# Kernel tuning notes

Hardware: AMD Instinct MI355X
Metric: run time of the kernel (lower is better)

The kernel has to match this reference:

```python
import jax, jax.numpy as jnp
import numpy as np

VOCAB, DIM, B, S = 32000, 1024, 64, 512

def setup_inputs() -> dict:
    key = jax.random.key(0)
    ks = jax.random.split(key, 16)
    std = 1.0 / np.sqrt(DIM)
    return {
        "x": jax.random.randint(ks[0], (B,), 0, VOCAB),
        "h": jax.random.normal(ks[1], (B, DIM), jnp.float32),
        "c": jax.random.normal(ks[2], (B, DIM), jnp.float32),
        "enc_y": jax.random.normal(ks[3], (B, S, DIM), jnp.float32),
        "F_emb": jax.random.normal(ks[4], (VOCAB, DIM), jnp.float32),
        "W1_w": jax.random.uniform(ks[5], (DIM, DIM), jnp.float32, -std, std),
        "W1_b": jnp.zeros((DIM,), jnp.float32),
        "W2_w": jax.random.uniform(ks[6], (DIM, DIM), jnp.float32, -std, std),
        "W2_b": jnp.zeros((DIM,), jnp.float32),
        "V_w": jax.random.uniform(ks[7], (1, DIM), jnp.float32, -std, std),
        "V_b": jnp.zeros((1,), jnp.float32),
        "W_ih": jax.random.uniform(ks[8], (4 * DIM, DIM), jnp.float32, -std, std),
        "W_hh": jax.random.uniform(ks[9], (4 * DIM, DIM), jnp.float32, -std, std),
        "b_ih": jax.random.uniform(ks[10], (4 * DIM,), jnp.float32, -std, std),
        "b_hh": jax.random.uniform(ks[11], (4 * DIM,), jnp.float32, -std, std),
        "fc_w": jax.random.uniform(ks[12], (VOCAB, DIM), jnp.float32, -std, std),
        "fc_b": jnp.zeros((VOCAB,), jnp.float32),
    }

def reference(x, h, c, enc_y, F_emb, W1_w, W1_b, W2_w, W2_b, V_w, V_b,
              W_ih, W_hh, b_ih, b_hh, fc_w, fc_b):
    # Bahdanau additive attention (weights returned; context is dead code for layer=1)
    i_s = jnp.einsum('bsd,ed->bse', enc_y, W1_w) + W1_b          # [B,S,D]
    j_s = (h @ W2_w.T + W2_b)[:, None, :]                        # [B,1,D]
    score = jnp.tanh(i_s + j_s)                                  # [B,S,D]
    att = jax.nn.softmax(score @ V_w.T + V_b, axis=1)            # [B,S,1]
    # embedding lookup for the step token
    emb = F_emb[x]                                               # [B,D]
    # single-step LSTM (pytorch gate order: i, f, g, o)
    gates = emb @ W_ih.T + b_ih + h @ W_hh.T + b_hh              # [B,4D]
    ig, fg, gg, og = jnp.split(gates, 4, axis=-1)
    c_new = jax.nn.sigmoid(fg) * c + jax.nn.sigmoid(ig) * jnp.tanh(gg)
    h_new = jax.nn.sigmoid(og) * jnp.tanh(c_new)
    out = h_new + emb                                            # residual skip
    logits = out @ fc_w.T + fc_b                                 # [B,VOCAB]
    return logits, h_new, c_new, att
```

## Files before the change

kernel.cpp:

```cpp
#include <hip/hip_runtime.h>

#define DEV __device__ __forceinline__

typedef __bf16 bf16_t;
typedef bf16_t bf16x8 __attribute__((ext_vector_type(8)));
typedef float f32x4 __attribute__((ext_vector_type(4)));

static constexpr int VOCAB = 32000, DIM = 1024, BATCH = 64, SEQ = 512;
static constexpr int M_SC = BATCH * SEQ;

DEV unsigned short f2bf(float f) {
  unsigned u = __builtin_bit_cast(unsigned, f);
  u += 0x7FFFu + ((u >> 16) & 1u);
  return (unsigned short)(u >> 16);
}

DEV float sigmf(float x) {
  x = fminf(fmaxf(x, -30.f), 30.f);
  return 1.0f / (1.0f + __expf(-x));
}

DEV float tanh_fast(float x) {
  x = fminf(fmaxf(x, -20.f), 20.f);
  float e = __expf(2.0f * x);
  return (e - 1.0f) / (e + 1.0f);
}

DEV void gload_lds16(const void* g, void* l) {
  __builtin_amdgcn_global_load_lds(
      (__attribute__((address_space(1))) void*)(g),
      (__attribute__((address_space(3))) void*)(l), 16, 0, 0);
}

__global__ void __launch_bounds__(256) k_prep(const float* __restrict__ enc,
                                              const float* __restrict__ w1,
                                              unsigned short* __restrict__ enc_b,
                                              unsigned short* __restrict__ w1_b,
                                              float* __restrict__ att_l) {
  int gid = blockIdx.x * 256 + threadIdx.x;
  if (gid < M_SC) att_l[gid] = 0.f;
  const int ENC4 = (M_SC * DIM) / 4;
  const int TOT4 = ENC4 + (DIM * DIM) / 4;
  int stride = gridDim.x * 256;
  for (int i = gid; i < TOT4; i += stride) {
    float4 v;
    unsigned short* dst;
    if (i < ENC4) {
      v = ((const float4*)enc)[i];
      dst = enc_b + (size_t)i * 4;
    } else {
      v = ((const float4*)w1)[i - ENC4];
      dst = w1_b + (size_t)(i - ENC4) * 4;
    }
    ushort4 o;
    o.x = f2bf(v.x); o.y = f2bf(v.y); o.z = f2bf(v.z); o.w = f2bf(v.w);
    *(ushort4*)dst = o;
  }
}

__global__ void k_embed(const int* __restrict__ x, const float* __restrict__ Femb,
                        const float* __restrict__ h, float* __restrict__ emb_f,
                        unsigned short* __restrict__ eh_b, unsigned short* __restrict__ h_b) {
  int b = blockIdx.x;
  int tok = x[b];
  for (int d = threadIdx.x; d < DIM; d += blockDim.x) {
    float e = Femb[(size_t)tok * DIM + d];
    float hv = h[b * DIM + d];
    emb_f[b * DIM + d] = e;
    unsigned short eb = f2bf(e), hb = f2bf(hv);
    eh_b[b * 2 * DIM + d] = eb;
    eh_b[b * 2 * DIM + DIM + d] = hb;
    h_b[b * DIM + d] = hb;
  }
}

__global__ void __launch_bounds__(256) k_skinny(
    const unsigned short* __restrict__ A, int lda,
    const float* __restrict__ B1, const float* __restrict__ B2, int ksplit,
    const float* __restrict__ bias, float* __restrict__ C, int N, int K) {
  __shared__ unsigned short As[2][64 * 128];
  __shared__ unsigned short Bs[2][16 * 128];
  int t = threadIdx.x;
  int l = t & 63, w = t >> 6;
  int n0 = blockIdx.x * 16;
  f32x4 acc = {};
  int rx = (l & 7) << 3;

  float4 vB[2];

  auto loadB = [&](int k0) {
    const float* Bsrc;
    int kk;
    if (k0 < ksplit) { Bsrc = B1; kk = k0; } else { Bsrc = B2; kk = k0 - ksplit; }
#pragma unroll
    for (int i = 0; i < 2; ++i) {
      int lin = i * 256 + t;
      int row = lin >> 5, c4 = (lin & 31) * 4;
      vB[i] = *(const float4*)(Bsrc + (size_t)(n0 + row) * 1024 + kk + c4);
    }
  };
  auto writeB = [&](int bufi) {
#pragma unroll
    for (int i = 0; i < 2; ++i) {
      int lin = i * 256 + t;
      int row = lin >> 5, c4 = (lin & 31) * 4;
      ushort4 o;
      o.x = f2bf(vB[i].x); o.y = f2bf(vB[i].y); o.z = f2bf(vB[i].z); o.w = f2bf(vB[i].w);
      *(ushort4*)&Bs[bufi][row * 128 + (c4 ^ ((row & 7) << 3))] = o;
    }
  };
  auto stageA = [&](int k0, int bufi) {
#pragma unroll
    for (int i = 0; i < 4; ++i) {
      int sbase = i * 256 + w * 64;
      int s = sbase + l;
      int row = s >> 4;
      int scol = ((s & 15) ^ (row & 7)) * 8;
      gload_lds16(A + (size_t)row * lda + k0 + scol, &As[bufi][sbase * 8]);
    }
  };
  auto compute = [&](int bufi) {
#pragma unroll
    for (int kf = 0; kf < 4; ++kf) {
      int ko = kf * 32 + 8 * (l >> 4);
      int ar = w * 16 + (l & 15);
      bf16x8 af = *(const bf16x8*)&As[bufi][ar * 128 + (ko ^ rx)];
      bf16x8 bf = *(const bf16x8*)&Bs[bufi][(l & 15) * 128 + (ko ^ rx)];
      acc = __builtin_amdgcn_mfma_f32_16x16x32_bf16(af, bf, acc, 0, 0, 0);
    }
  };

  loadB(0);
  stageA(0, 0);
  writeB(0);
  asm volatile("s_waitcnt lgkmcnt(0)" ::: "memory");

  int nk = K / 128;
  int cur = 0;
  for (int kt = 0; kt < nk - 1; ++kt) {
    loadB((kt + 1) * 128);
    stageA((kt + 1) * 128, cur ^ 1);
    asm volatile("s_waitcnt vmcnt(6)\n\ts_barrier" ::: "memory");
    compute(cur);
    writeB(cur ^ 1);
    asm volatile("s_waitcnt lgkmcnt(0)\n\ts_barrier" ::: "memory");
    cur ^= 1;
  }
  asm volatile("s_waitcnt vmcnt(0)\n\ts_barrier" ::: "memory");
  compute(cur);

  int cn = n0 + (l & 15);
  float bv = bias ? bias[cn] : 0.f;
#pragma unroll
  for (int r = 0; r < 4; ++r) {
    int m = w * 16 + (l >> 4) * 4 + r;
    C[(size_t)m * N + cn] = acc[r] + bv;
  }
}

__global__ void __launch_bounds__(256) k_score(
    const unsigned short* __restrict__ encb, const unsigned short* __restrict__ w1mat,
    const float* __restrict__ js, const float* __restrict__ w1bias,
    const float* __restrict__ vw, float* __restrict__ att_l) {
  __shared__ unsigned short As[2][128 * 64];
  __shared__ unsigned short Bs[2][128 * 64];
  int t = threadIdx.x;
  int l = t & 63, w = t >> 6;
  int wr = w >> 1, wc = w & 1;
  int wg = blockIdx.x;
  int swz = (wg & 7) * 256 + (wg >> 3);
  int m0 = (swz >> 3) * 128;
  int n0 = (swz & 7) * 128;
  f32x4 acc[4][4] = {};

  int srow = l >> 3;
  int scol = ((l & 7) ^ (l >> 3)) * 8;
  int rx = (l & 7) << 3;

  const unsigned short* pa = encb + (size_t)m0 * DIM;
  const unsigned short* pb = w1mat + (size_t)n0 * DIM;

  auto stage = [&](int kt, int bufi) {
    int kbase = kt * 64;
#pragma unroll
    for (int i = 0; i < 4; ++i) {
      int chunk = i * 4 + w;
      int row = chunk * 8 + srow;
      gload_lds16(pa + (size_t)row * DIM + kbase + scol, &As[bufi][chunk * 512]);
      gload_lds16(pb + (size_t)row * DIM + kbase + scol, &Bs[bufi][chunk * 512]);
    }
  };
  auto compute = [&](int bufi) {
#pragma unroll
    for (int kh = 0; kh < 2; ++kh) {
      int ko = kh * 32 + 8 * (l >> 4);
      int kos = ko ^ rx;
      bf16x8 bfr[4], afr[4];
#pragma unroll
      for (int ni = 0; ni < 4; ++ni)
        bfr[ni] = *(const bf16x8*)&Bs[bufi][(wc * 64 + ni * 16 + (l & 15)) * 64 + kos];
#pragma unroll
      for (int mi = 0; mi < 4; ++mi)
        afr[mi] = *(const bf16x8*)&As[bufi][(wr * 64 + mi * 16 + (l & 15)) * 64 + kos];
      __builtin_amdgcn_s_setprio(1);
#pragma unroll
      for (int mi = 0; mi < 4; ++mi)
#pragma unroll
        for (int ni = 0; ni < 4; ++ni)
          acc[mi][ni] = __builtin_amdgcn_mfma_f32_16x16x32_bf16(afr[mi], bfr[ni], acc[mi][ni], 0, 0, 0);
      __builtin_amdgcn_s_setprio(0);
    }
  };

  stage(0, 0);
  int cur = 0;
  for (int kt = 0; kt < 15; ++kt) {
    stage(kt + 1, cur ^ 1);
    asm volatile("s_waitcnt vmcnt(8)\n\ts_barrier" ::: "memory");
    compute(cur);
    asm volatile("s_barrier" ::: "memory");
    cur ^= 1;
  }
  asm volatile("s_waitcnt vmcnt(0)\n\ts_barrier" ::: "memory");
  compute(cur);

  int b = m0 >> 9;
  const float* jrow = js + b * DIM;
  float psum[4][4] = {};
#pragma unroll
  for (int ni = 0; ni < 4; ++ni) {
    int e = n0 + wc * 64 + ni * 16 + (l & 15);
    float jv = jrow[e] + w1bias[e];
    float vv = vw[e];
#pragma unroll
    for (int mi = 0; mi < 4; ++mi)
#pragma unroll
      for (int r = 0; r < 4; ++r)
        psum[mi][r] += tanh_fast(acc[mi][ni][r] + jv) * vv;
  }
#pragma unroll
  for (int mi = 0; mi < 4; ++mi)
#pragma unroll
    for (int r = 0; r < 4; ++r) {
      float s = psum[mi][r];
      s += __shfl_xor(s, 1);
      s += __shfl_xor(s, 2);
      s += __shfl_xor(s, 4);
      s += __shfl_xor(s, 8);
      if ((l & 15) == 0)
        atomicAdd(&att_l[m0 + wr * 64 + mi * 16 + (l >> 4) * 4 + r], s);
    }
}

__global__ void k_softmax(const float* __restrict__ att_l, float* __restrict__ att) {
  __shared__ float red[16];
  int b = blockIdx.x, t = threadIdx.x;
  float v = att_l[b * SEQ + t];
  float m = v;
#pragma unroll
  for (int o = 32; o; o >>= 1) m = fmaxf(m, __shfl_xor(m, o));
  if ((t & 63) == 0) red[t >> 6] = m;
  __syncthreads();
  m = red[0];
#pragma unroll
  for (int i = 1; i < 8; ++i) m = fmaxf(m, red[i]);
  float e = __expf(v - m);
  float s = e;
#pragma unroll
  for (int o = 32; o; o >>= 1) s += __shfl_xor(s, o);
  __syncthreads();
  if ((t & 63) == 0) red[8 + (t >> 6)] = s;
  __syncthreads();
  s = 0.f;
#pragma unroll
  for (int i = 0; i < 8; ++i) s += red[8 + i];
  att[b * SEQ + t] = e / s;
}

__global__ void k_lstm(const float* __restrict__ gates, const float* __restrict__ bih,
                       const float* __restrict__ bhh, const float* __restrict__ c,
                       const float* __restrict__ emb_f, float* __restrict__ out_h,
                       float* __restrict__ out_c, unsigned short* __restrict__ out_b) {
  int t = blockIdx.x * 256 + threadIdx.x;
  int b = t >> 10, d = t & 1023;
  const float* g = gates + b * 4 * DIM;
  float ig = g[d] + bih[d] + bhh[d];
  float fg = g[DIM + d] + bih[DIM + d] + bhh[DIM + d];
  float gg = g[2 * DIM + d] + bih[2 * DIM + d] + bhh[2 * DIM + d];
  float og = g[3 * DIM + d] + bih[3 * DIM + d] + bhh[3 * DIM + d];
  float cn = sigmf(fg) * c[t] + sigmf(ig) * tanh_fast(gg);
  float hn = sigmf(og) * tanh_fast(cn);
  out_h[t] = hn;
  out_c[t] = cn;
  out_b[t] = f2bf(hn + emb_f[t]);
}

extern "C" void kernel_launch(void* const* d_in, const int* in_sizes, int n_in,
                              void* d_out, int out_size, void* d_ws, size_t ws_size,
                              hipStream_t stream) {
  const int* x = (const int*)d_in[0];
  const float* h = (const float*)d_in[1];
  const float* c = (const float*)d_in[2];
  const float* enc = (const float*)d_in[3];
  const float* Femb = (const float*)d_in[4];
  const float* W1w = (const float*)d_in[5];
  const float* W1b = (const float*)d_in[6];
  const float* W2w = (const float*)d_in[7];
  const float* W2b = (const float*)d_in[8];
  const float* Vw = (const float*)d_in[9];
  const float* Wih = (const float*)d_in[11];
  const float* Whh = (const float*)d_in[12];
  const float* bih = (const float*)d_in[13];
  const float* bhh = (const float*)d_in[14];
  const float* fcw = (const float*)d_in[15];
  const float* fcb = (const float*)d_in[16];

  float* out_logits = (float*)d_out;
  float* out_h = out_logits + (size_t)BATCH * VOCAB;
  float* out_c = out_h + BATCH * DIM;
  float* out_att = out_c + BATCH * DIM;

  char* p = (char*)d_ws;
  unsigned short* enc_b = (unsigned short*)p; p += (size_t)M_SC * DIM * 2;
  unsigned short* w1_b = (unsigned short*)p;  p += (size_t)DIM * DIM * 2;
  float* att_l = (float*)p;                   p += (size_t)M_SC * 4;
  float* js = (float*)p;                      p += (size_t)BATCH * DIM * 4;
  float* emb_f = (float*)p;                   p += (size_t)BATCH * DIM * 4;
  unsigned short* eh_b = (unsigned short*)p;  p += (size_t)BATCH * 2 * DIM * 2;
  unsigned short* h_b = (unsigned short*)p;   p += (size_t)BATCH * DIM * 2;
  float* gates = (float*)p;                   p += (size_t)BATCH * 4 * DIM * 4;
  unsigned short* out_b = (unsigned short*)p; p += (size_t)BATCH * DIM * 2;

  hipLaunchKernelGGL(k_prep, dim3(2048), dim3(256), 0, stream, enc, W1w, enc_b, w1_b, att_l);
  hipLaunchKernelGGL(k_embed, dim3(BATCH), dim3(256), 0, stream, x, Femb, h, emb_f, eh_b, h_b);
  hipLaunchKernelGGL(k_skinny, dim3(DIM / 16), dim3(256), 0, stream,
                     h_b, DIM, W2w, W2w, DIM, W2b, js, DIM, DIM);
  hipLaunchKernelGGL(k_score, dim3(2048), dim3(256), 0, stream,
                     enc_b, w1_b, js, W1b, Vw, att_l);
  hipLaunchKernelGGL(k_softmax, dim3(BATCH), dim3(SEQ), 0, stream, att_l, out_att);
  hipLaunchKernelGGL(k_skinny, dim3(4 * DIM / 16), dim3(256), 0, stream,
                     eh_b, 2 * DIM, Wih, Whh, DIM, (const float*)nullptr, gates, 4 * DIM, 2 * DIM);
  hipLaunchKernelGGL(k_lstm, dim3(BATCH * DIM / 256), dim3(256), 0, stream,
                     gates, bih, bhh, c, emb_f, out_h, out_c, out_b);
  hipLaunchKernelGGL(k_skinny, dim3(VOCAB / 16), dim3(256), 0, stream,
                     out_b, DIM, fcw, fcw, DIM, fcb, out_logits, VOCAB, DIM);
}
```

Measured before the change: 201.9 us.

## Fuse fp32-to-bf16 conversion of encoder states into score GEMM A-tile loads

The separate pass that converted the whole 32768x1024 encoder tensor to bf16 in workspace is removed. The score kernel now loads fp32 encoder rows into registers, converts them, and writes swizzled bf16 into LDS, software-pipelined one k-step ahead. The tile grows to 128x256 with 512 threads, so each fp32 A row is read from HBM four times instead of eight times as bf16. This saves the write and re-read of a 64MB intermediate, at the cost of more register pressure and VALU conversion work inside the GEMM loop.

```diff
diff --git a/kernel.cpp b/kernel.cpp
--- a/kernel.cpp
+++ b/kernel.cpp
@@ -32,30 +32,15 @@
       (__attribute__((address_space(3))) void*)(l), 16, 0, 0);
 }
 
-__global__ void __launch_bounds__(256) k_prep(const float* __restrict__ enc,
-                                              const float* __restrict__ w1,
-                                              unsigned short* __restrict__ enc_b,
-                                              unsigned short* __restrict__ w1_b,
-                                              float* __restrict__ att_l) {
+__global__ void __launch_bounds__(256) k_small(const float* __restrict__ w1,
+                                               unsigned short* __restrict__ w1_b,
+                                               float* __restrict__ att_l) {
   int gid = blockIdx.x * 256 + threadIdx.x;
   if (gid < M_SC) att_l[gid] = 0.f;
-  const int ENC4 = (M_SC * DIM) / 4;
-  const int TOT4 = ENC4 + (DIM * DIM) / 4;
-  int stride = gridDim.x * 256;
-  for (int i = gid; i < TOT4; i += stride) {
-    float4 v;
-    unsigned short* dst;
-    if (i < ENC4) {
-      v = ((const float4*)enc)[i];
-      dst = enc_b + (size_t)i * 4;
-    } else {
-      v = ((const float4*)w1)[i - ENC4];
-      dst = w1_b + (size_t)(i - ENC4) * 4;
-    }
-    ushort4 o;
-    o.x = f2bf(v.x); o.y = f2bf(v.y); o.z = f2bf(v.z); o.w = f2bf(v.w);
-    *(ushort4*)dst = o;
-  }
+  float4 v = ((const float4*)w1)[gid];
+  ushort4 o;
+  o.x = f2bf(v.x); o.y = f2bf(v.y); o.z = f2bf(v.z); o.w = f2bf(v.w);
+  *(ushort4*)(w1_b + (size_t)gid * 4) = o;
 }
 
 __global__ void k_embed(const int* __restrict__ x, const float* __restrict__ Femb,
@@ -158,97 +143,127 @@
   }
 }
 
-__global__ void __launch_bounds__(256) k_score(
-    const unsigned short* __restrict__ encb, const unsigned short* __restrict__ w1mat,
+__global__ void __launch_bounds__(512) k_score(
+    const float* __restrict__ enc, const unsigned short* __restrict__ w1mat,
     const float* __restrict__ js, const float* __restrict__ w1bias,
     const float* __restrict__ vw, float* __restrict__ att_l) {
   __shared__ unsigned short As[2][128 * 64];
-  __shared__ unsigned short Bs[2][128 * 64];
-  int t = threadIdx.x;
-  int l = t & 63, w = t >> 6;
-  int wr = w >> 1, wc = w & 1;
+  __shared__ unsigned short Bs[2][256 * 64];
+  int tid = threadIdx.x;
+  int lane = tid & 63, wid = tid >> 6;
+  int wr = wid >> 2, wn = wid & 3;
+  int lm = lane & 15, lq = lane >> 4;
+  int rx = (lane & 7) << 3;
+
   int wg = blockIdx.x;
-  int swz = (wg & 7) * 256 + (wg >> 3);
-  int m0 = (swz >> 3) * 128;
-  int n0 = (swz & 7) * 128;
+  int swz = (wg & 7) * 128 + (wg >> 3);
+  int m0 = (swz >> 2) * 128;
+  int n0 = (swz & 3) * 256;
+
   f32x4 acc[4][4] = {};
 
-  int srow = l >> 3;
-  int scol = ((l & 7) ^ (l >> 3)) * 8;
-  int rx = (l & 7) << 3;
-
-  const unsigned short* pa = encb + (size_t)m0 * DIM;
-  const unsigned short* pb = w1mat + (size_t)n0 * DIM;
-
-  auto stage = [&](int kt, int bufi) {
-    int kbase = kt * 64;
+  int arow[2], aq[2];
+#pragma unroll
+  for (int i = 0; i < 2; ++i) {
+    int lin = i * 512 + tid;
+    arow[i] = lin >> 3;
+    aq[i] = lin & 7;
+  }
+  float4 vA[2][2];
+  auto loadA = [&](int kb) {
+#pragma unroll
+    for (int i = 0; i < 2; ++i) {
+      const float* src = enc + (size_t)(m0 + arow[i]) * DIM + kb + aq[i] * 8;
+      vA[i][0] = *(const float4*)(src);
+      vA[i][1] = *(const float4*)(src + 4);
+    }
+  };
+  auto writeA = [&](int bufi) {
+#pragma unroll
+    for (int i = 0; i < 2; ++i) {
+      uint4 o;
+      o.x = (unsigned)f2bf(vA[i][0].x) | ((unsigned)f2bf(vA[i][0].y) << 16);
+      o.y = (unsigned)f2bf(vA[i][0].z) | ((unsigned)f2bf(vA[i][0].w) << 16);
+      o.z = (unsigned)f2bf(vA[i][1].x) | ((unsigned)f2bf(vA[i][1].y) << 16);
+      o.w = (unsigned)f2bf(vA[i][1].z) | ((unsigned)f2bf(vA[i][1].w) << 16);
+      *(uint4*)&As[bufi][arow[i] * 64 + ((aq[i] ^ (arow[i] & 7)) * 8)] = o;
+    }
+  };
+  auto stageB = [&](int kb, int bufi) {
 #pragma unroll
     for (int i = 0; i < 4; ++i) {
-      int chunk = i * 4 + w;
-      int row = chunk * 8 + srow;
-      gload_lds16(pa + (size_t)row * DIM + kbase + scol, &As[bufi][chunk * 512]);
-      gload_lds16(pb + (size_t)row * DIM + kbase + scol, &Bs[bufi][chunk * 512]);
+      int sbase = i * 512 + wid * 64;
+      int s = sbase + lane;
+      int brow = s >> 3, bq = s & 7;
+      int bcol = (bq ^ (brow & 7)) * 8;
+      gload_lds16(w1mat + (size_t)(n0 + brow) * DIM + kb + bcol, &Bs[bufi][sbase * 8]);
     }
   };
   auto compute = [&](int bufi) {
 #pragma unroll
-    for (int kh = 0; kh < 2; ++kh) {
-      int ko = kh * 32 + 8 * (l >> 4);
-      int kos = ko ^ rx;
-      bf16x8 bfr[4], afr[4];
-#pragma unroll
-      for (int ni = 0; ni < 4; ++ni)
-        bfr[ni] = *(const bf16x8*)&Bs[bufi][(wc * 64 + ni * 16 + (l & 15)) * 64 + kos];
-#pragma unroll
-      for (int mi = 0; mi < 4; ++mi)
-        afr[mi] = *(const bf16x8*)&As[bufi][(wr * 64 + mi * 16 + (l & 15)) * 64 + kos];
+    for (int kf = 0; kf < 2; ++kf) {
+      int kos = (kf * 32 + 8 * lq) ^ rx;
+      bf16x8 af[4], bfr[4];
+#pragma unroll
+      for (int mf = 0; mf < 4; ++mf)
+        af[mf] = *(const bf16x8*)&As[bufi][(wr * 64 + mf * 16 + lm) * 64 + kos];
+#pragma unroll
+      for (int nf = 0; nf < 4; ++nf)
+        bfr[nf] = *(const bf16x8*)&Bs[bufi][(wn * 64 + nf * 16 + lm) * 64 + kos];
       __builtin_amdgcn_s_setprio(1);
 #pragma unroll
-      for (int mi = 0; mi < 4; ++mi)
-#pragma unroll
-        for (int ni = 0; ni < 4; ++ni)
-          acc[mi][ni] = __builtin_amdgcn_mfma_f32_16x16x32_bf16(afr[mi], bfr[ni], acc[mi][ni], 0, 0, 0);
+      for (int mf = 0; mf < 4; ++mf)
+#pragma unroll
+        for (int nf = 0; nf < 4; ++nf)
+          acc[mf][nf] = __builtin_amdgcn_mfma_f32_16x16x32_bf16(af[mf], bfr[nf], acc[mf][nf], 0, 0, 0);
       __builtin_amdgcn_s_setprio(0);
     }
   };
 
-  stage(0, 0);
-  int cur = 0;
-  for (int kt = 0; kt < 15; ++kt) {
-    stage(kt + 1, cur ^ 1);
-    asm volatile("s_waitcnt vmcnt(8)\n\ts_barrier" ::: "memory");
-    compute(cur);
-    asm volatile("s_barrier" ::: "memory");
-    cur ^= 1;
-  }
-  asm volatile("s_waitcnt vmcnt(0)\n\ts_barrier" ::: "memory");
-  compute(cur);
+  loadA(0);
+  stageB(0, 0);
+  writeA(0);
+  asm volatile("s_waitcnt lgkmcnt(0)\n\ts_barrier" ::: "memory");
+
+  for (int t = 0; t < 16; ++t) {
+    int s = t & 1;
+    if (t < 15) {
+      loadA((t + 1) * 64);
+      stageB((t + 1) * 64, s ^ 1);
+      asm volatile("s_waitcnt vmcnt(8)\n\ts_barrier" ::: "memory");
+    } else {
+      asm volatile("s_waitcnt vmcnt(0)\n\ts_barrier" ::: "memory");
+    }
+    compute(s);
+    if (t < 15) writeA(s ^ 1);
+    asm volatile("s_waitcnt lgkmcnt(0)\n\ts_barrier" ::: "memory");
+  }
 
   int b = m0 >> 9;
   const float* jrow = js + b * DIM;
   float psum[4][4] = {};
 #pragma unroll
-  for (int ni = 0; ni < 4; ++ni) {
-    int e = n0 + wc * 64 + ni * 16 + (l & 15);
+  for (int nf = 0; nf < 4; ++nf) {
+    int e = n0 + wn * 64 + nf * 16 + lm;
     float jv = jrow[e] + w1bias[e];
     float vv = vw[e];
 #pragma unroll
-    for (int mi = 0; mi < 4; ++mi)
+    for (int mf = 0; mf < 4; ++mf)
 #pragma unroll
       for (int r = 0; r < 4; ++r)
-        psum[mi][r] += tanh_fast(acc[mi][ni][r] + jv) * vv;
-  }
-#pragma unroll
-  for (int mi = 0; mi < 4; ++mi)
+        psum[mf][r] += tanh_fast(acc[mf][nf][r] + jv) * vv;
+  }
+#pragma unroll
+  for (int mf = 0; mf < 4; ++mf)
 #pragma unroll
     for (int r = 0; r < 4; ++r) {
-      float s = psum[mi][r];
+      float s = psum[mf][r];
       s += __shfl_xor(s, 1);
       s += __shfl_xor(s, 2);
       s += __shfl_xor(s, 4);
       s += __shfl_xor(s, 8);
-      if ((l & 15) == 0)
-        atomicAdd(&att_l[m0 + wr * 64 + mi * 16 + (l >> 4) * 4 + r], s);
+      if (lm == 0)
+        atomicAdd(&att_l[m0 + wr * 64 + mf * 16 + lq * 4 + r], s);
     }
 }
 
@@ -321,7 +336,6 @@
   float* out_att = out_c + BATCH * DIM;
 
   char* p = (char*)d_ws;
-  unsigned short* enc_b = (unsigned short*)p; p += (size_t)M_SC * DIM * 2;
   unsigned short* w1_b = (unsigned short*)p;  p += (size_t)DIM * DIM * 2;
   float* att_l = (float*)p;                   p += (size_t)M_SC * 4;
   float* js = (float*)p;                      p += (size_t)BATCH * DIM * 4;
@@ -331,12 +345,13 @@
   float* gates = (float*)p;                   p += (size_t)BATCH * 4 * DIM * 4;
   unsigned short* out_b = (unsigned short*)p; p += (size_t)BATCH * DIM * 2;
 
-  hipLaunchKernelGGL(k_prep, dim3(2048), dim3(256), 0, stream, enc, W1w, enc_b, w1_b, att_l);
+  hipLaunchKernelGGL(k_small, dim3(DIM * DIM / 4 / 256), dim3(256), 0, stream,
+                     W1w, w1_b, att_l);
   hipLaunchKernelGGL(k_embed, dim3(BATCH), dim3(256), 0, stream, x, Femb, h, emb_f, eh_b, h_b);
   hipLaunchKernelGGL(k_skinny, dim3(DIM / 16), dim3(256), 0, stream,
                      h_b, DIM, W2w, W2w, DIM, W2b, js, DIM, DIM);
-  hipLaunchKernelGGL(k_score, dim3(2048), dim3(256), 0, stream,
-                     enc_b, w1_b, js, W1b, Vw, att_l);
+  hipLaunchKernelGGL(k_score, dim3(1024), dim3(512), 0, stream,
+                     enc, w1_b, js, W1b, Vw, att_l);
   hipLaunchKernelGGL(k_softmax, dim3(BATCH), dim3(SEQ), 0, stream, att_l, out_att);
   hipLaunchKernelGGL(k_skinny, dim3(4 * DIM / 16), dim3(256), 0, stream,
                      eh_b, 2 * DIM, Wih, Whh, DIM, (const float*)nullptr, gates, 4 * DIM, 2 * DIM);
```

Result: slower. 235.8 us (+16.8%).

## Enlarge score GEMM tile to 256x256 with 8 waves and quadrant-interleaved pipeline

Applied to the files above, without the earlier changes.

Rewrites the attention score GEMM to use 256x256 output tiles computed by 512 threads (8 waves, each with a 128x64 sub-tile), replacing the 128x128 tiles on 256 threads. The K-loop is split into four quadrant MFMA phases, with the next tile's A and B half-loads interleaved between them so global-to-LDS copies overlap compute. The aim is to raise arithmetic intensity and cut redundant global and LDS traffic. In exchange it uses more registers and LDS (128 KB double buffered), which may limit occupancy, and the grid drops to 512 blocks, which can hurt load balance.

```diff
diff --git a/kernel.cpp b/kernel.cpp
--- a/kernel.cpp
+++ b/kernel.cpp
@@ -158,99 +158,152 @@
   }
 }
 
-__global__ void __launch_bounds__(256) k_score(
+#define READ_A(MH)                                                              \
+  do {                                                                          \
+    _Pragma("unroll") for (int mf = 0; mf < 4; ++mf)                            \
+    _Pragma("unroll") for (int kk = 0; kk < 2; ++kk) {                          \
+      int row_ = wm * 128 + (MH) * 64 + mf * 16 + lm;                           \
+      fa[mf][kk] = *(const bf16x8*)&As[ct][row_ * 64 + ((kk * 32 + 8 * lq) ^ rx)]; \
+    }                                                                           \
+  } while (0)
+#define READ_B(NH)                                                              \
+  do {                                                                          \
+    _Pragma("unroll") for (int nf = 0; nf < 2; ++nf)                            \
+    _Pragma("unroll") for (int kk = 0; kk < 2; ++kk) {                          \
+      int row_ = wn * 64 + (NH) * 32 + nf * 16 + lm;                            \
+      fb[NH][nf][kk] = *(const bf16x8*)&Bs[ct][row_ * 64 + ((kk * 32 + 8 * lq) ^ rx)]; \
+    }                                                                           \
+  } while (0)
+#define MFMA_Q(MH, NH)                                                          \
+  do {                                                                          \
+    __builtin_amdgcn_s_setprio(1);                                              \
+    _Pragma("unroll") for (int mf = 0; mf < 4; ++mf)                            \
+    _Pragma("unroll") for (int nf = 0; nf < 2; ++nf)                            \
+    _Pragma("unroll") for (int kk = 0; kk < 2; ++kk)                            \
+        acc[(MH) * 4 + mf][(NH) * 2 + nf] = __builtin_amdgcn_mfma_f32_16x16x32_bf16( \
+            fa[mf][kk], fb[NH][nf][kk], acc[(MH) * 4 + mf][(NH) * 2 + nf], 0, 0, 0); \
+    __builtin_amdgcn_s_setprio(0);                                              \
+  } while (0)
+
+__global__ void __launch_bounds__(512, 2) k_score(
     const unsigned short* __restrict__ encb, const unsigned short* __restrict__ w1mat,
     const float* __restrict__ js, const float* __restrict__ w1bias,
     const float* __restrict__ vw, float* __restrict__ att_l) {
-  __shared__ unsigned short As[2][128 * 64];
-  __shared__ unsigned short Bs[2][128 * 64];
-  int t = threadIdx.x;
-  int l = t & 63, w = t >> 6;
-  int wr = w >> 1, wc = w & 1;
+  __shared__ unsigned short As[2][256 * 64];
+  __shared__ unsigned short Bs[2][256 * 64];
+  int tid = threadIdx.x;
+  int lane = tid & 63, wid = tid >> 6;
+  int wm = wid >> 2, wn = wid & 3;
+  int lm = lane & 15, lq = lane >> 4;
+  int rx = (lane & 7) << 3;
+
   int wg = blockIdx.x;
-  int swz = (wg & 7) * 256 + (wg >> 3);
-  int m0 = (swz >> 3) * 128;
-  int n0 = (swz & 7) * 128;
-  f32x4 acc[4][4] = {};
-
-  int srow = l >> 3;
-  int scol = ((l & 7) ^ (l >> 3)) * 8;
-  int rx = (l & 7) << 3;
+  int swz = (wg & 7) * 64 + (wg >> 3);
+  int m0 = (swz >> 2) * 256;
+  int n0 = (swz & 3) * 256;
 
   const unsigned short* pa = encb + (size_t)m0 * DIM;
   const unsigned short* pb = w1mat + (size_t)n0 * DIM;
 
-  auto stage = [&](int kt, int bufi) {
-    int kbase = kt * 64;
-#pragma unroll
-    for (int i = 0; i < 4; ++i) {
-      int chunk = i * 4 + w;
-      int row = chunk * 8 + srow;
-      gload_lds16(pa + (size_t)row * DIM + kbase + scol, &As[bufi][chunk * 512]);
-      gload_lds16(pb + (size_t)row * DIM + kbase + scol, &Bs[bufi][chunk * 512]);
-    }
-  };
-  auto compute = [&](int bufi) {
-#pragma unroll
-    for (int kh = 0; kh < 2; ++kh) {
-      int ko = kh * 32 + 8 * (l >> 4);
-      int kos = ko ^ rx;
-      bf16x8 bfr[4], afr[4];
-#pragma unroll
-      for (int ni = 0; ni < 4; ++ni)
-        bfr[ni] = *(const bf16x8*)&Bs[bufi][(wc * 64 + ni * 16 + (l & 15)) * 64 + kos];
-#pragma unroll
-      for (int mi = 0; mi < 4; ++mi)
-        afr[mi] = *(const bf16x8*)&As[bufi][(wr * 64 + mi * 16 + (l & 15)) * 64 + kos];
-      __builtin_amdgcn_s_setprio(1);
-#pragma unroll
-      for (int mi = 0; mi < 4; ++mi)
-#pragma unroll
-        for (int ni = 0; ni < 4; ++ni)
-          acc[mi][ni] = __builtin_amdgcn_mfma_f32_16x16x32_bf16(afr[mi], bfr[ni], acc[mi][ni], 0, 0, 0);
-      __builtin_amdgcn_s_setprio(0);
-    }
-  };
-
-  stage(0, 0);
-  int cur = 0;
-  for (int kt = 0; kt < 15; ++kt) {
-    stage(kt + 1, cur ^ 1);
-    asm volatile("s_waitcnt vmcnt(8)\n\ts_barrier" ::: "memory");
-    compute(cur);
-    asm volatile("s_barrier" ::: "memory");
-    cur ^= 1;
-  }
-  asm volatile("s_waitcnt vmcnt(0)\n\ts_barrier" ::: "memory");
-  compute(cur);
+  f32x4 acc[8][4] = {};
+  bf16x8 fa[4][2];
+  bf16x8 fb[2][2][2];
+
+  auto stageA = [&](int kt, int h, int bufi) {
+#pragma unroll
+    for (int i = 0; i < 2; ++i) {
+      int rowbase = i * 128 + h * 64 + wid * 8;
+      int row = rowbase + (lane >> 3);
+      int scol = ((lane & 7) ^ (row & 7)) * 8;
+      gload_lds16(pa + (size_t)row * DIM + kt * 64 + scol, &As[bufi][rowbase * 64]);
+    }
+  };
+  auto stageB = [&](int kt, int h, int bufi) {
+#pragma unroll
+    for (int i = 0; i < 2; ++i) {
+      int j0 = i * 64 + wid * 8;
+      int rowbase = (j0 >> 5) * 64 + h * 32 + (j0 & 31);
+      int row = rowbase + (lane >> 3);
+      int scol = ((lane & 7) ^ (row & 7)) * 8;
+      gload_lds16(pb + (size_t)row * DIM + kt * 64 + scol, &Bs[bufi][rowbase * 64]);
+    }
+  };
+
+  stageA(0, 0, 0);
+  stageB(0, 0, 0);
+  stageB(0, 1, 0);
+  stageA(0, 1, 0);
+  asm volatile("s_waitcnt vmcnt(4)\n\ts_barrier" ::: "memory");
+
+  for (int t = 0; t < 15; ++t) {
+    const int ct = t & 1;
+    READ_A(0); READ_B(0);
+    stageA(t + 1, 0, ct ^ 1);
+    asm volatile("s_waitcnt vmcnt(4)\n\ts_barrier" ::: "memory");
+    MFMA_Q(0, 0);
+    asm volatile("s_barrier" ::: "memory");
+    READ_B(1);
+    stageB(t + 1, 0, ct ^ 1);
+    asm volatile("s_waitcnt vmcnt(4)\n\ts_barrier" ::: "memory");
+    MFMA_Q(0, 1);
+    asm volatile("s_barrier" ::: "memory");
+    READ_A(1);
+    stageB(t + 1, 1, ct ^ 1);
+    asm volatile("s_barrier" ::: "memory");
+    MFMA_Q(1, 1);
+    asm volatile("s_barrier" ::: "memory");
+    stageA(t + 1, 1, ct ^ 1);
+    asm volatile("s_waitcnt vmcnt(4)\n\ts_barrier" ::: "memory");
+    MFMA_Q(1, 0);
+    asm volatile("s_barrier" ::: "memory");
+  }
+  {
+    const int ct = 1;
+    READ_A(0); READ_B(0);
+    asm volatile("s_waitcnt vmcnt(2)\n\ts_barrier" ::: "memory");
+    MFMA_Q(0, 0);
+    asm volatile("s_barrier" ::: "memory");
+    READ_B(1);
+    asm volatile("s_waitcnt vmcnt(0)\n\ts_barrier" ::: "memory");
+    MFMA_Q(0, 1);
+    asm volatile("s_barrier" ::: "memory");
+    READ_A(1);
+    MFMA_Q(1, 1);
+    MFMA_Q(1, 0);
+  }
 
   int b = m0 >> 9;
   const float* jrow = js + b * DIM;
-  float psum[4][4] = {};
-#pragma unroll
-  for (int ni = 0; ni < 4; ++ni) {
-    int e = n0 + wc * 64 + ni * 16 + (l & 15);
-    float jv = jrow[e] + w1bias[e];
-    float vv = vw[e];
-#pragma unroll
-    for (int mi = 0; mi < 4; ++mi)
+  float jvv[4], vvv[4];
+#pragma unroll
+  for (int nj = 0; nj < 4; ++nj) {
+    int e = n0 + wn * 64 + nj * 16 + lm;
+    jvv[nj] = jrow[e] + w1bias[e];
+    vvv[nj] = vw[e];
+  }
+#pragma unroll
+  for (int mi = 0; mi < 8; ++mi) {
+    float psum[4] = {0.f, 0.f, 0.f, 0.f};
+#pragma unroll
+    for (int nj = 0; nj < 4; ++nj)
 #pragma unroll
       for (int r = 0; r < 4; ++r)
-        psum[mi][r] += tanh_fast(acc[mi][ni][r] + jv) * vv;
-  }
-#pragma unroll
-  for (int mi = 0; mi < 4; ++mi)
+        psum[r] += tanh_fast(acc[mi][nj][r] + jvv[nj]) * vvv[nj];
 #pragma unroll
     for (int r = 0; r < 4; ++r) {
-      float s = psum[mi][r];
+      float s = psum[r];
       s += __shfl_xor(s, 1);
       s += __shfl_xor(s, 2);
       s += __shfl_xor(s, 4);
       s += __shfl_xor(s, 8);
-      if ((l & 15) == 0)
-        atomicAdd(&att_l[m0 + wr * 64 + mi * 16 + (l >> 4) * 4 + r], s);
-    }
-}
+      if (lm == 0)
+        atomicAdd(&att_l[m0 + wm * 128 + mi * 16 + lq * 4 + r], s);
+    }
+  }
+}
+#undef READ_A
+#undef READ_B
+#undef MFMA_Q
 
 __global__ void k_softmax(const float* __restrict__ att_l, float* __restrict__ att) {
   __shared__ float red[16];
@@ -335,7 +388,7 @@
   hipLaunchKernelGGL(k_embed, dim3(BATCH), dim3(256), 0, stream, x, Femb, h, emb_f, eh_b, h_b);
   hipLaunchKernelGGL(k_skinny, dim3(DIM / 16), dim3(256), 0, stream,
                      h_b, DIM, W2w, W2w, DIM, W2b, js, DIM, DIM);
-  hipLaunchKernelGGL(k_score, dim3(2048), dim3(256), 0, stream,
+  hipLaunchKernelGGL(k_score, dim3(512), dim3(512), 0, stream,
                      enc_b, w1_b, js, W1b, Vw, att_l);
   hipLaunchKernelGGL(k_softmax, dim3(BATCH), dim3(SEQ), 0, stream, att_l, out_att);
   hipLaunchKernelGGL(k_skinny, dim3(4 * DIM / 16), dim3(256), 0, stream,
```

Measured after the change: 184.8 us. 1.09x faster.
